# Performance work log

Hardware: AMD Instinct MI355X
Metric: run time of the kernel (lower is better)

## Reference

```python
import jax, jax.numpy as jnp
import numpy as np

N_NODES = 100000
N_EDGES = 1600000
IN_C, HID_C, OUT_C = 128, 64, 64


def setup_inputs() -> dict:
    key = jax.random.key(0)
    ks = jax.random.split(key, 9)
    x = jax.random.normal(ks[0], (N_NODES, IN_C), dtype=jnp.float32)
    src = jax.random.randint(ks[1], (N_EDGES,), 0, N_NODES, dtype=jnp.int64)
    dst = jax.random.randint(ks[2], (N_EDGES,), 0, N_NODES, dtype=jnp.int64)
    # Glorot-ish init for linear weights
    W1 = jax.random.normal(ks[3], (IN_C, HID_C), dtype=jnp.float32) / np.sqrt(IN_C)
    b1 = jnp.zeros((HID_C,), dtype=jnp.float32)
    W2 = jax.random.normal(ks[4], (HID_C, HID_C), dtype=jnp.float32) / np.sqrt(HID_C)
    b2 = jnp.zeros((HID_C,), dtype=jnp.float32)
    W3 = jax.random.normal(ks[5], (HID_C, OUT_C), dtype=jnp.float32) / np.sqrt(HID_C)
    b3 = jnp.zeros((OUT_C,), dtype=jnp.float32)
    return {"x": x, "src": src, "dst": dst,
            "W1": W1, "b1": b1, "W2": W2, "b2": b2, "W3": W3, "b3": b3}


def _gcn_conv(x, src, dst, W, b):
    # GCNConv(normalize=False): out = A @ (x W) + b  (unweighted sum aggregation)
    h = x @ W                          # [N, d_out] dense transform first (d_out small)
    msg = h[src]                       # gather per edge: [E, d_out]
    agg = jax.ops.segment_sum(msg, dst, num_segments=N_NODES)  # scatter-add
    return agg + b


def reference(x, src, dst, W1, b1, W2, b2, W3, b3):
    # layer 1..num_layers-1: conv -> activation -> dropout(eval: no-op)
    h = jax.nn.relu(_gcn_conv(x, src, dst, W1, b1))
    h = jax.nn.relu(_gcn_conv(h, src, dst, W2, b2))
    # last layer: conv -> activation
    out = jax.nn.relu(_gcn_conv(h, src, dst, W3, b3))
    return out
```

## Files before the change

kernel.cpp:

```cpp
#include <hip/hip_runtime.h>

#define N_NODES_C 100000
#define N_EDGES_C 1600000
#define NCHUNK 256
#define CHH (N_EDGES_C / NCHUNK)
#define NPART 128
#define CHP (N_EDGES_C / NPART)
#define BUCK_SH 7
#define BUCK_NODES 128
#define NB_BUCK 782

typedef short short8 __attribute__((ext_vector_type(8)));
typedef float f32x4 __attribute__((ext_vector_type(4)));
typedef float f32x2 __attribute__((ext_vector_type(2)));

__device__ __forceinline__ short f2bf(float f) {
  unsigned u = __builtin_bit_cast(unsigned, f);
  unsigned r = (u + 0x7FFFu + ((u >> 16) & 1u)) >> 16;
  return (short)r;
}

__device__ __forceinline__ unsigned char f32_to_fp8_hw(float x) {
  return (unsigned char)(__builtin_amdgcn_cvt_pk_fp8_f32(x, x, 0, false) & 0xFF);
}

template <int K>
__device__ __forceinline__ void gemm64_body(
    int gblock, const float* __restrict__ in_, const float* __restrict__ W,
    unsigned char* __restrict__ out_, int n_rows) {
  constexpr int KS = K / 32;
  int wave = threadIdx.x >> 6;
  int lane = threadIdx.x & 63;
  int row0 = (gblock * 4 + wave) * 16;
  if (row0 >= n_rows) return;

  int lrow = lane & 15;
  int lk = (lane >> 4) * 8;

  short8 bfrag[KS][4];
#pragma unroll
  for (int ks = 0; ks < KS; ++ks)
#pragma unroll
    for (int nt = 0; nt < 4; ++nt) {
      short8 b;
#pragma unroll
      for (int j = 0; j < 8; ++j)
        b[j] = f2bf(W[(size_t)(ks * 32 + lk + j) * 64 + nt * 16 + lrow]);
      bfrag[ks][nt] = b;
    }

  int row = row0 + lrow;
  f32x4 acc[4] = {};
#pragma unroll
  for (int ks = 0; ks < KS; ++ks) {
    short8 a;
    const float* ip = in_ + (size_t)row * K + ks * 32 + lk;
    f32x4 v0 = *(const f32x4*)(ip);
    f32x4 v1 = *(const f32x4*)(ip + 4);
#pragma unroll
    for (int j = 0; j < 4; ++j) {
      a[j] = f2bf(v0[j]);
      a[4 + j] = f2bf(v1[j]);
    }
#pragma unroll
    for (int nt = 0; nt < 4; ++nt)
      acc[nt] = __builtin_amdgcn_mfma_f32_16x16x32_bf16(a, bfrag[ks][nt],
                                                        acc[nt], 0, 0, 0);
  }

  int crow = row0 + (lane >> 4) * 4;
#pragma unroll
  for (int nt = 0; nt < 4; ++nt) {
    int ocol = nt * 16 + lrow;
#pragma unroll
    for (int r = 0; r < 4; ++r)
      out_[(size_t)(crow + r) * 64 + ocol] = f32_to_fp8_hw(acc[nt][r]);
  }
}

__global__ __launch_bounds__(256) void hist_kernel(
    const int* __restrict__ dst, int* __restrict__ countsT) {
  __shared__ int lhist[NB_BUCK];
  int cb = (int)blockIdx.x;
  for (int i = threadIdx.x; i < NB_BUCK; i += 256) lhist[i] = 0;
  __syncthreads();
  int beg = cb * CHH, end = beg + CHH;
  for (int i = beg + (int)threadIdx.x; i < end; i += 256)
    atomicAdd(&lhist[((unsigned)dst[i]) >> BUCK_SH], 1);
  __syncthreads();
  for (int bb = threadIdx.x; bb < NB_BUCK; bb += 256)
    countsT[bb * NCHUNK + cb] = lhist[bb];
}

__global__ __launch_bounds__(256) void scan_buckets_kernel(
    int* __restrict__ countsT, int* __restrict__ btot) {
  int b = blockIdx.x * 4 + (threadIdx.x >> 6);
  int lane = threadIdx.x & 63;
  if (b >= NB_BUCK) return;
  int4 v = *(const int4*)(countsT + b * NCHUNK + lane * 4);
  int s = v.x + v.y + v.z + v.w;
  int incl = s;
#pragma unroll
  for (int d = 1; d < 64; d <<= 1) {
    int t = __shfl_up(incl, d, 64);
    if (lane >= d) incl += t;
  }
  int excl = incl - s;
  int4 o;
  o.x = excl;
  o.y = excl + v.x;
  o.z = o.y + v.y;
  o.w = o.z + v.z;
  *(int4*)(countsT + b * NCHUNK + lane * 4) = o;
  if (lane == 63) btot[b] = incl;
}

__global__ __launch_bounds__(1024) void scan_btot_kernel(
    const int* __restrict__ btot, int* __restrict__ bstart) {
  __shared__ int lds[1024];
  int t = threadIdx.x;
  int v = (t < NB_BUCK) ? btot[t] : 0;
  lds[t] = v;
  __syncthreads();
  for (int off = 1; off < 1024; off <<= 1) {
    int tv = (t >= off) ? lds[t - off] : 0;
    __syncthreads();
    lds[t] += tv;
    __syncthreads();
  }
  if (t < NB_BUCK) bstart[t] = lds[t] - v;
  if (t == NB_BUCK - 1) bstart[NB_BUCK] = lds[t];
}

__global__ __launch_bounds__(256) void part_gemm1_kernel(
    const int* __restrict__ src, const int* __restrict__ dst,
    const int* __restrict__ offs ,
    const int* __restrict__ bstart, unsigned* __restrict__ packed,
    const float* __restrict__ x, const float* __restrict__ W1,
    unsigned char* __restrict__ hA, int n_rows) {
  __shared__ int cur[NB_BUCK];
  int b = (int)blockIdx.x;
  if (b >= NPART) {
    gemm64_body<128>(b - NPART, x, W1, hA, n_rows);
    return;
  }
  for (int bb = threadIdx.x; bb < NB_BUCK; bb += 256)
    cur[bb] = bstart[bb] + offs[bb * NCHUNK + 2 * b];
  __syncthreads();
  int beg = b * CHP, end = beg + CHP;
  for (int i = beg + (int)threadIdx.x; i < end; i += 256) {
    int d = dst[i];
    int s = src[i];
    int bb = ((unsigned)d) >> BUCK_SH;
    int pos = atomicAdd(&cur[bb], 1);
    packed[pos] = ((unsigned)(d & (BUCK_NODES - 1)) << 17) | (unsigned)s;
  }
}

__global__ __launch_bounds__(256) void sort_bucket_kernel(
    const unsigned* __restrict__ packed, const int* __restrict__ bstart,
    int* __restrict__ col, int* __restrict__ row_ptr, int n_nodes,
    int n_edges) {
  __shared__ int lhist[BUCK_NODES];
  __shared__ int lcur[BUCK_NODES];
  __shared__ int wsum0;
  int b = (int)blockIdx.x;
  int beg = bstart[b], end = bstart[b + 1];
  int t = (int)threadIdx.x;

  if (t < BUCK_NODES) lhist[t] = 0;
  __syncthreads();
  for (int e = beg + t; e < end; e += 256)
    atomicAdd(&lhist[packed[e] >> 17], 1);
  __syncthreads();

  int v = 0, incl = 0;
  if (t < BUCK_NODES) {
    v = lhist[t];
    incl = v;
#pragma unroll
    for (int d = 1; d < 64; d <<= 1) {
      int u = __shfl_up(incl, d, 64);
      if ((t & 63) >= d) incl += u;
    }
  }
  if (t == 63) wsum0 = incl;
  __syncthreads();
  if (t >= 64 && t < BUCK_NODES) incl += wsum0;
  if (t < BUCK_NODES) {
    int excl = incl - v;
    lcur[t] = excl;
    int node = b * BUCK_NODES + t;
    if (node < n_nodes) row_ptr[node] = beg + excl;
  }
  if (b == NB_BUCK - 1 && t == 0) row_ptr[n_nodes] = n_edges;
  __syncthreads();

  for (int e = beg + t; e < end; e += 256) {
    unsigned pe = packed[e];
    int ld = (int)(pe >> 17);
    int pos = beg + atomicAdd(&lcur[ld], 1);
    col[pos] = (int)(pe & 0x1FFFFu);
  }
}

__device__ __forceinline__ void agg_node(
    const unsigned char* __restrict__ h, const int* __restrict__ col, int beg,
    int end, int slot, int q, float& s0, float& s1, float& s2, float& s3) {
  s0 = s1 = s2 = s3 = 0.f;
  float t0 = 0.f, t1 = 0.f, t2 = 0.f, t3 = 0.f;
  int e = beg + slot;
  for (; e + 12 < end; e += 16) {
    int sa = col[e];
    int sb = col[e + 4];
    int sc = col[e + 8];
    int sd = col[e + 12];
    int ua = *(const int*)(h + (size_t)sa * 64 + q * 4);
    int ub = *(const int*)(h + (size_t)sb * 64 + q * 4);
    int uc = *(const int*)(h + (size_t)sc * 64 + q * 4);
    int ud = *(const int*)(h + (size_t)sd * 64 + q * 4);
    f32x2 al = __builtin_amdgcn_cvt_pk_f32_fp8(ua, false);
    f32x2 ah = __builtin_amdgcn_cvt_pk_f32_fp8(ua, true);
    f32x2 bl = __builtin_amdgcn_cvt_pk_f32_fp8(ub, false);
    f32x2 bh = __builtin_amdgcn_cvt_pk_f32_fp8(ub, true);
    f32x2 cl = __builtin_amdgcn_cvt_pk_f32_fp8(uc, false);
    f32x2 ch = __builtin_amdgcn_cvt_pk_f32_fp8(uc, true);
    f32x2 dl = __builtin_amdgcn_cvt_pk_f32_fp8(ud, false);
    f32x2 dh = __builtin_amdgcn_cvt_pk_f32_fp8(ud, true);
    s0 += al[0] + bl[0];
    s1 += al[1] + bl[1];
    s2 += ah[0] + bh[0];
    s3 += ah[1] + bh[1];
    t0 += cl[0] + dl[0];
    t1 += cl[1] + dl[1];
    t2 += ch[0] + dh[0];
    t3 += ch[1] + dh[1];
  }
  for (; e < end; e += 4) {
    int sa = col[e];
    int ua = *(const int*)(h + (size_t)sa * 64 + q * 4);
    f32x2 al = __builtin_amdgcn_cvt_pk_f32_fp8(ua, false);
    f32x2 ah = __builtin_amdgcn_cvt_pk_f32_fp8(ua, true);
    s0 += al[0];
    s1 += al[1];
    s2 += ah[0];
    s3 += ah[1];
  }
  s0 += t0;
  s1 += t1;
  s2 += t2;
  s3 += t3;
  s0 += __shfl_xor(s0, 16);
  s1 += __shfl_xor(s1, 16);
  s2 += __shfl_xor(s2, 16);
  s3 += __shfl_xor(s3, 16);
  s0 += __shfl_xor(s0, 32);
  s1 += __shfl_xor(s1, 32);
  s2 += __shfl_xor(s2, 32);
  s3 += __shfl_xor(s3, 32);
}

__global__ __launch_bounds__(256) void agg_gemm_kernel(
    const unsigned char* __restrict__ h, const int* __restrict__ row_ptr,
    const int* __restrict__ col, const float* __restrict__ bias,
    const float* __restrict__ W, unsigned char* __restrict__ outg,
    int n_nodes) {
  __shared__ float rowbuf[16][68];
  int wid = threadIdx.x >> 6;
  int lane = threadIdx.x & 63;
  int slot = lane >> 4;
  int q = lane & 15;
  int nbase = blockIdx.x * 16;

#pragma unroll
  for (int n = 0; n < 4; ++n) {
    int ln = wid * 4 + n;
    int node = nbase + ln;
    float s0, s1, s2, s3;
    agg_node(h, col, row_ptr[node], row_ptr[node + 1], slot, q, s0, s1, s2, s3);
    if (lane < 16) {
      f32x4 r;
      r[0] = fmaxf(s0 + bias[q * 4 + 0], 0.f);
      r[1] = fmaxf(s1 + bias[q * 4 + 1], 0.f);
      r[2] = fmaxf(s2 + bias[q * 4 + 2], 0.f);
      r[3] = fmaxf(s3 + bias[q * 4 + 3], 0.f);
      *(f32x4*)&rowbuf[ln][q * 4] = r;
    }
  }
  __syncthreads();

  int lrow = lane & 15;
  int lk = (lane >> 4) * 8;
  f32x4 acc = {};
#pragma unroll
  for (int ks = 0; ks < 2; ++ks) {
    short8 a, bv;
#pragma unroll
    for (int j = 0; j < 8; ++j) a[j] = f2bf(rowbuf[lrow][ks * 32 + lk + j]);
#pragma unroll
    for (int j = 0; j < 8; ++j)
      bv[j] = f2bf(W[(size_t)(ks * 32 + lk + j) * 64 + wid * 16 + lrow]);
    acc = __builtin_amdgcn_mfma_f32_16x16x32_bf16(a, bv, acc, 0, 0, 0);
  }
  int crow = (lane >> 4) * 4;
#pragma unroll
  for (int r = 0; r < 4; ++r)
    outg[(size_t)(nbase + crow + r) * 64 + wid * 16 + lrow] =
        f32_to_fp8_hw(acc[r]);
}

__global__ __launch_bounds__(256) void agg_final_kernel(
    const unsigned char* __restrict__ h, const int* __restrict__ row_ptr,
    const int* __restrict__ col, const float* __restrict__ bias,
    float* __restrict__ out, int n_nodes) {
  int node = blockIdx.x * 4 + (threadIdx.x >> 6);
  if (node >= n_nodes) return;
  int lane = threadIdx.x & 63;
  int slot = lane >> 4;
  int q = lane & 15;
  float s0, s1, s2, s3;
  agg_node(h, col, row_ptr[node], row_ptr[node + 1], slot, q, s0, s1, s2, s3);
  if (lane < 16) {
    float4 v;
    v.x = fmaxf(s0 + bias[q * 4 + 0], 0.f);
    v.y = fmaxf(s1 + bias[q * 4 + 1], 0.f);
    v.z = fmaxf(s2 + bias[q * 4 + 2], 0.f);
    v.w = fmaxf(s3 + bias[q * 4 + 3], 0.f);
    ((float4*)out)[(size_t)node * 16 + q] = v;
  }
}

extern "C" void kernel_launch(void* const* d_in, const int* in_sizes, int n_in,
                              void* d_out, int out_size, void* d_ws,
                              size_t ws_size, hipStream_t stream) {
  const float* x = (const float*)d_in[0];
  const int* src = (const int*)d_in[1];
  const int* dst = (const int*)d_in[2];
  const float* W1 = (const float*)d_in[3];
  const float* b1 = (const float*)d_in[4];
  const float* W2 = (const float*)d_in[5];
  const float* b2 = (const float*)d_in[6];
  const float* W3 = (const float*)d_in[7];
  const float* b3 = (const float*)d_in[8];
  float* out = (float*)d_out;

  const int N = N_NODES_C;
  const int E = N_EDGES_C;

  char* ws = (char*)d_ws;
  int* countsT = (int*)(ws + 0);
  int* btot = (int*)(ws + (1u << 20));
  int* bstart = (int*)(ws + (1u << 20) + (16u << 10));
  int* row_ptr = (int*)(ws + (2u << 20));
  unsigned* packed = (unsigned*)(ws + (3u << 20));
  int* col = (int*)(ws + (10u << 20));
  unsigned char* hA = (unsigned char*)(ws + (17u << 20));
  unsigned char* hB = (unsigned char*)(ws + (24u << 20));

  const int gemm_grid = (N + 63) / 64;
  const int k1_grid = (NB_BUCK + 3) / 4;
  const int aggg_grid = N / 16;
  const int aggf_grid = (N + 3) / 4;

  hist_kernel<<<NCHUNK, 256, 0, stream>>>(dst, countsT);
  scan_buckets_kernel<<<k1_grid, 256, 0, stream>>>(countsT, btot);
  scan_btot_kernel<<<1, 1024, 0, stream>>>(btot, bstart);
  part_gemm1_kernel<<<NPART + gemm_grid, 256, 0, stream>>>(
      src, dst, countsT, bstart, packed, x, W1, hA, N);
  sort_bucket_kernel<<<NB_BUCK, 256, 0, stream>>>(packed, bstart, col, row_ptr,
                                                  N, E);

  agg_gemm_kernel<<<aggg_grid, 256, 0, stream>>>(hA, row_ptr, col, b1, W2, hB,
                                                 N);
  agg_gemm_kernel<<<aggg_grid, 256, 0, stream>>>(hB, row_ptr, col, b2, W3, hA,
                                                 N);
  agg_final_kernel<<<aggf_grid, 256, 0, stream>>>(hA, row_ptr, col, b3, out, N);
}
```

Before: 209.3 us.

## Fuse first GEMM into histogram kernel, widen partition blocks, use nontemporal accesses

The layer-1 dense transform now runs as extra blocks of the histogram kernel instead of the partition kernel. The partition kernel runs on its own with 1024-thread blocks. Nontemporal loads are used for col indices in aggregation, and nontemporal stores for the fp8 hidden outputs and the final output. The goal is to overlap the GEMM with the lighter histogram pass, shorten the partition step, and keep streaming data from displacing gathered features in cache. The catch is that the h buffers written nontemporally are gathered again by the next layer, so they may miss in cache.

```diff
diff --git a/kernel.cpp b/kernel.cpp
--- a/kernel.cpp
+++ b/kernel.cpp
@@ -78,18 +78,24 @@
   }
 }
 
-__global__ __launch_bounds__(256) void hist_kernel(
-    const int* __restrict__ dst, int* __restrict__ countsT) {
+__global__ __launch_bounds__(256) void hist_gemm1_kernel(
+    const int* __restrict__ dst, int* __restrict__ countsT,
+    const float* __restrict__ x, const float* __restrict__ W1,
+    unsigned char* __restrict__ hA, int n_rows) {
   __shared__ int lhist[NB_BUCK];
-  int cb = (int)blockIdx.x;
+  int b = (int)blockIdx.x;
+  if (b >= NCHUNK) {
+    gemm64_body<128>(b - NCHUNK, x, W1, hA, n_rows);
+    return;
+  }
   for (int i = threadIdx.x; i < NB_BUCK; i += 256) lhist[i] = 0;
   __syncthreads();
-  int beg = cb * CHH, end = beg + CHH;
+  int beg = b * CHH, end = beg + CHH;
   for (int i = beg + (int)threadIdx.x; i < end; i += 256)
     atomicAdd(&lhist[((unsigned)dst[i]) >> BUCK_SH], 1);
   __syncthreads();
   for (int bb = threadIdx.x; bb < NB_BUCK; bb += 256)
-    countsT[bb * NCHUNK + cb] = lhist[bb];
+    countsT[bb * NCHUNK + b] = lhist[bb];
 }
 
 __global__ __launch_bounds__(256) void scan_buckets_kernel(
@@ -132,23 +138,17 @@
   if (t == NB_BUCK - 1) bstart[NB_BUCK] = lds[t];
 }
 
-__global__ __launch_bounds__(256) void part_gemm1_kernel(
+__global__ __launch_bounds__(1024) void partition_kernel(
     const int* __restrict__ src, const int* __restrict__ dst,
     const int* __restrict__ offs ,
-    const int* __restrict__ bstart, unsigned* __restrict__ packed,
-    const float* __restrict__ x, const float* __restrict__ W1,
-    unsigned char* __restrict__ hA, int n_rows) {
+    const int* __restrict__ bstart, unsigned* __restrict__ packed) {
   __shared__ int cur[NB_BUCK];
   int b = (int)blockIdx.x;
-  if (b >= NPART) {
-    gemm64_body<128>(b - NPART, x, W1, hA, n_rows);
-    return;
-  }
-  for (int bb = threadIdx.x; bb < NB_BUCK; bb += 256)
+  for (int bb = threadIdx.x; bb < NB_BUCK; bb += 1024)
     cur[bb] = bstart[bb] + offs[bb * NCHUNK + 2 * b];
   __syncthreads();
   int beg = b * CHP, end = beg + CHP;
-  for (int i = beg + (int)threadIdx.x; i < end; i += 256) {
+  for (int i = beg + (int)threadIdx.x; i < end; i += 1024) {
     int d = dst[i];
     int s = src[i];
     int bb = ((unsigned)d) >> BUCK_SH;
@@ -211,10 +211,10 @@
   float t0 = 0.f, t1 = 0.f, t2 = 0.f, t3 = 0.f;
   int e = beg + slot;
   for (; e + 12 < end; e += 16) {
-    int sa = col[e];
-    int sb = col[e + 4];
-    int sc = col[e + 8];
-    int sd = col[e + 12];
+    int sa = __builtin_nontemporal_load(col + e);
+    int sb = __builtin_nontemporal_load(col + e + 4);
+    int sc = __builtin_nontemporal_load(col + e + 8);
+    int sd = __builtin_nontemporal_load(col + e + 12);
     int ua = *(const int*)(h + (size_t)sa * 64 + q * 4);
     int ub = *(const int*)(h + (size_t)sb * 64 + q * 4);
     int uc = *(const int*)(h + (size_t)sc * 64 + q * 4);
@@ -237,7 +237,7 @@
     t3 += ch[1] + dh[1];
   }
   for (; e < end; e += 4) {
-    int sa = col[e];
+    int sa = __builtin_nontemporal_load(col + e);
     int ua = *(const int*)(h + (size_t)sa * 64 + q * 4);
     f32x2 al = __builtin_amdgcn_cvt_pk_f32_fp8(ua, false);
     f32x2 ah = __builtin_amdgcn_cvt_pk_f32_fp8(ua, true);
@@ -305,8 +305,9 @@
   int crow = (lane >> 4) * 4;
 #pragma unroll
   for (int r = 0; r < 4; ++r)
-    outg[(size_t)(nbase + crow + r) * 64 + wid * 16 + lrow] =
-        f32_to_fp8_hw(acc[r]);
+    __builtin_nontemporal_store(
+        f32_to_fp8_hw(acc[r]),
+        outg + (size_t)(nbase + crow + r) * 64 + wid * 16 + lrow);
 }
 
 __global__ __launch_bounds__(256) void agg_final_kernel(
@@ -321,12 +322,12 @@
   float s0, s1, s2, s3;
   agg_node(h, col, row_ptr[node], row_ptr[node + 1], slot, q, s0, s1, s2, s3);
   if (lane < 16) {
-    float4 v;
-    v.x = fmaxf(s0 + bias[q * 4 + 0], 0.f);
-    v.y = fmaxf(s1 + bias[q * 4 + 1], 0.f);
-    v.z = fmaxf(s2 + bias[q * 4 + 2], 0.f);
-    v.w = fmaxf(s3 + bias[q * 4 + 3], 0.f);
-    ((float4*)out)[(size_t)node * 16 + q] = v;
+    f32x4 v;
+    v[0] = fmaxf(s0 + bias[q * 4 + 0], 0.f);
+    v[1] = fmaxf(s1 + bias[q * 4 + 1], 0.f);
+    v[2] = fmaxf(s2 + bias[q * 4 + 2], 0.f);
+    v[3] = fmaxf(s3 + bias[q * 4 + 3], 0.f);
+    __builtin_nontemporal_store(v, (f32x4*)out + (size_t)node * 16 + q);
   }
 }
 
@@ -362,11 +363,12 @@
   const int aggg_grid = N / 16;
   const int aggf_grid = (N + 3) / 4;
 
-  hist_kernel<<<NCHUNK, 256, 0, stream>>>(dst, countsT);
+  hist_gemm1_kernel<<<NCHUNK + gemm_grid, 256, 0, stream>>>(dst, countsT, x,
+                                                            W1, hA, N);
   scan_buckets_kernel<<<k1_grid, 256, 0, stream>>>(countsT, btot);
   scan_btot_kernel<<<1, 1024, 0, stream>>>(btot, bstart);
-  part_gemm1_kernel<<<NPART + gemm_grid, 256, 0, stream>>>(
-      src, dst, countsT, bstart, packed, x, W1, hA, N);
+  partition_kernel<<<NPART, 1024, 0, stream>>>(src, dst, countsT, bstart,
+                                               packed);
   sort_bucket_kernel<<<NB_BUCK, 256, 0, stream>>>(packed, bstart, col, row_ptr,
                                                   N, E);
 
```

After: 226.5 us. +8.2%, slower.
